# Optimization experiments

Measured on AMD Instinct MI355X. Metric: run time of the kernel, lower is better.

## Reference

```python
import jax, jax.numpy as jnp
import numpy as np

B, S, D, H = 2, 2048, 2048, 16
HD = D // H  # 128


def _rope_tables(seq_len, half_dim, theta=10000.0):
    freqs = 1.0 / (theta ** (np.arange(0, half_dim, dtype=np.float32) / half_dim))
    t = np.arange(seq_len, dtype=np.float32)
    ang = np.outer(t, freqs)  # [S, HD//2]
    return jnp.asarray(np.cos(ang)), jnp.asarray(np.sin(ang))


def setup_inputs() -> dict:
    key = jax.random.key(0)
    kx, kq, kk, kv, ko = jax.random.split(key, 5)
    cos, sin = _rope_tables(S, HD // 2)
    return {
        "x": jax.random.normal(kx, (B, S, D), dtype=jnp.float32),
        "cos": cos,  # [S, HD//2]
        "sin": sin,  # [S, HD//2]
        "wq": jax.random.normal(kq, (D, D), dtype=jnp.float32) * 0.02,
        "wk": jax.random.normal(kk, (D, D), dtype=jnp.float32) * 0.02,
        "wv": jax.random.normal(kv, (D, D), dtype=jnp.float32) * 0.02,
        "wo": jax.random.normal(ko, (D, D), dtype=jnp.float32) * 0.02,
    }


def _apply_rotary(t, cos, sin):
    # t: [B, S, H, HD]; rotate consecutive pairs (complex multiply)
    t2 = t.reshape(*t.shape[:-1], HD // 2, 2)
    te, to = t2[..., 0], t2[..., 1]
    c = cos[None, :, None, :]
    s = sin[None, :, None, :]
    out = jnp.stack([te * c - to * s, te * s + to * c], axis=-1)
    return out.reshape(t.shape)


def reference(x, cos, sin, wq, wk, wv, wo):
    xq = (x @ wq).reshape(B, S, H, HD)
    xk = (x @ wk).reshape(B, S, H, HD)
    xv = (x @ wv).reshape(B, S, H, HD)
    # FAITHFUL to source: rotary applied to xq and xv (NOT xk)
    xq = _apply_rotary(xq, cos, sin)
    xv = _apply_rotary(xv, cos, sin)
    q = xq.transpose(0, 2, 1, 3)  # [B,H,S,HD]
    k = xk.transpose(0, 2, 1, 3)
    v = xv.transpose(0, 2, 1, 3)
    scores = jnp.einsum("bhqd,bhkd->bhqk", q, k) / jnp.sqrt(jnp.float32(HD))
    mask = jnp.triu(jnp.full((S, S), -jnp.inf, dtype=scores.dtype), k=1)
    scores = scores + mask[None, None, :, :]
    probs = jax.nn.softmax(scores, axis=-1)
    out = jnp.einsum("bhqk,bhkd->bhqd", probs, v)  # [B,H,S,HD]
    out = out.transpose(0, 2, 1, 3).reshape(B, S, D)
    return out @ wo
```

## Files before the change

### kernel.cpp

```cpp
#include <hip/hip_runtime.h>
#include <hip/hip_bf16.h>

typedef short short8 __attribute__((ext_vector_type(8)));
typedef float f32x4 __attribute__((ext_vector_type(4)));
typedef int int4v __attribute__((ext_vector_type(4)));

#define B_ 2
#define S_ 2048
#define D_ 2048
#define H_ 16
#define HD_ 128
#define K_ 2048

#define GLL16(gp, lp) __builtin_amdgcn_global_load_lds( \
    (const __attribute__((address_space(1))) void*)(gp), \
    (__attribute__((address_space(3))) void*)(lp), 16, 0, 0)

__device__ inline ushort f2bf(float f) {
    union { float f; unsigned u; } v; v.f = f;
    unsigned r = v.u + 0x7FFFu + ((v.u >> 16) & 1u);
    return (ushort)(r >> 16);
}
__device__ inline float bf2f(ushort b) {
    union { unsigned u; float f; } v; v.u = ((unsigned)b) << 16;
    return v.f;
}

__global__ void cast_kernel(const float* __restrict__ src, ushort* __restrict__ dst, int n4) {
    int i = blockIdx.x * blockDim.x + threadIdx.x;
    if (i >= n4) return;
    float4 v = reinterpret_cast<const float4*>(src)[i];
    ushort4 o;
    o.x = f2bf(v.x); o.y = f2bf(v.y); o.z = f2bf(v.z); o.w = f2bf(v.w);
    reinterpret_cast<ushort4*>(dst)[i] = o;
}

__global__ __launch_bounds__(256) void cast_transpose4(
        const float* __restrict__ s0, const float* __restrict__ s1,
        const float* __restrict__ s2, const float* __restrict__ s3,
        ushort* __restrict__ d0, ushort* __restrict__ d1,
        ushort* __restrict__ d2, ushort* __restrict__ d3) {
    __shared__ ushort tile[64][72];
    const int z = blockIdx.z;
    const float* src = (z == 0) ? s0 : (z == 1) ? s1 : (z == 2) ? s2 : s3;
    ushort* dst = (z == 0) ? d0 : (z == 1) ? d1 : (z == 2) ? d2 : d3;
    const int bk = blockIdx.y * 64, bn = blockIdx.x * 64;
    const int t = threadIdx.x;
    #pragma unroll
    for (int it = 0; it < 4; ++it) {
        int id = t + it * 256;
        int row = id >> 4;
        int c4 = (id & 15) * 4;
        float4 v = *reinterpret_cast<const float4*>(&src[(size_t)(bk + row) * D_ + bn + c4]);
        ushort4 o; o.x = f2bf(v.x); o.y = f2bf(v.y); o.z = f2bf(v.z); o.w = f2bf(v.w);
        *reinterpret_cast<ushort4*>(&tile[row][c4]) = o;
    }
    __syncthreads();
    #pragma unroll
    for (int it = 0; it < 4; ++it) {
        int id = t + it * 256;
        int n = id >> 4;
        int c4 = (id & 15) * 4;
        ushort4 o;
        o.x = tile[c4 + 0][n]; o.y = tile[c4 + 1][n];
        o.z = tile[c4 + 2][n]; o.w = tile[c4 + 3][n];
        *reinterpret_cast<ushort4*>(&dst[(size_t)(bn + n) * D_ + bk + c4]) = o;
    }
}

__global__ void rope_kernel(ushort* __restrict__ t, const float* __restrict__ cosT,
                            const float* __restrict__ sinT, int npairs) {
    int pid = blockIdx.x * blockDim.x + threadIdx.x;
    if (pid >= npairs) return;
    int i = pid & 63;
    int s = (pid >> 6) & (S_ - 1);
    unsigned pr = reinterpret_cast<unsigned*>(t)[pid];
    float e = bf2f((ushort)(pr & 0xFFFFu));
    float o = bf2f((ushort)(pr >> 16));
    float c = cosT[s * 64 + i];
    float sn = sinT[s * 64 + i];
    float oe = e * c - o * sn;
    float oo = e * sn + o * c;
    unsigned outp = ((unsigned)f2bf(oo) << 16) | (unsigned)f2bf(oe);
    reinterpret_cast<unsigned*>(t)[pid] = outp;
}

#define BAR8() __builtin_amdgcn_s_barrier()
#define VMC1() asm volatile("s_waitcnt vmcnt(1)" ::: "memory")
#define VMC0() asm volatile("s_waitcnt vmcnt(0)" ::: "memory")

template<int MODE>
__global__ __launch_bounds__(512, 2) void gemm8(const ushort* __restrict__ A,
        const ushort* __restrict__ Bt, ushort* __restrict__ q0, ushort* __restrict__ k0,
        ushort* __restrict__ v0, float* __restrict__ outf, int nbx) {
    constexpr int NC      = (MODE == 0) ? 3 : 2;
    constexpr int BN      = (MODE == 0) ? 192 : 128;
    constexpr int WCOLS   = BN / 4;
    constexpr int BBYTES  = BN * 128;
    constexpr int BSTRIDE = 32768 + BBYTES;

    extern __shared__ char smem[];
    const int tid = threadIdx.x, lane = tid & 63, wv = tid >> 6;
    const int wm = wv >> 2, wn = wv & 3;
    const int l15 = lane & 15, lg = lane >> 4;
    const int nwg = (int)gridDim.x, cpx = nwg >> 3;
    const int swzb = ((int)blockIdx.x & 7) * cpx + ((int)blockIdx.x >> 3);
    const int bn = (swzb % nbx) * BN, bm = (swzb / nbx) * 256;

    f32x4 acc[8][NC] = {};

    const int grl = wv * 8 + (lane >> 3);
    const int swc = (((lane & 7) ^ ((lane >> 3) & 7)) * 8);
    const ushort* Ag = A + (size_t)(bm + grl) * K_ + swc;
    const ushort* Bg = Bt + (size_t)(bn + grl) * K_ + swc;
    const size_t rowHA = (size_t)128 * K_;
    const size_t row64 = (size_t)64 * K_;

#define STAGE_A(t, h) do { if ((t) < 32) { \
        const ushort* g = Ag + (size_t)(h) * rowHA + (size_t)(t) * 64; \
        char* l = smem + (((t) & 1) ? BSTRIDE : 0) + ((h) << 14) + (wv << 10); \
        GLL16(g, l); GLL16(g + row64, l + 8192); } } while (0)
#define STAGE_B(t, ch) do { if ((t) < 32) { \
        const ushort* g = Bg + (size_t)(ch) * row64 + (size_t)(t) * 64; \
        char* l = smem + (((t) & 1) ? BSTRIDE : 0) + 32768 + (ch) * 8192 + (wv << 10); \
        GLL16(g, l); } } while (0)
#define STAGE_B_HI(t) do { STAGE_B(t, 1); if (MODE == 0) STAGE_B(t, 2); } while (0)

    const int colsw0 = (lg * 16) ^ ((l15 & 7) << 4);
    const int colsw1 = (64 + lg * 16) ^ ((l15 & 7) << 4);
    const char* abase0 = smem + (wm << 14);
    const char* bbase0 = smem + 32768;
    const char* abase1 = abase0 + BSTRIDE;
    const char* bbase1 = bbase0 + BSTRIDE;

#define LDA(ab, q, cs) do { _Pragma("unroll") for (int f = 0; f < 4; ++f) \
        a[f] = *reinterpret_cast<const short8*>((ab) + ((q) * 64 + f * 16 + l15) * 128 + (cs)); } while (0)
#define LDB(bb, cs) do { _Pragma("unroll") for (int c = 0; c < NC; ++c) { \
        const int rw = wn * WCOLS + c * 16; \
        b[c] = *reinterpret_cast<const short8*>((bb) + (rw >> 6) * 8192 + ((rw & 63) + l15) * 128 + (cs)); } } while (0)
#define MM(q) do { __builtin_amdgcn_s_setprio(1); \
        _Pragma("unroll") for (int f = 0; f < 4; ++f) \
        _Pragma("unroll") for (int c = 0; c < NC; ++c) \
            acc[(q) * 4 + f][c] = __builtin_amdgcn_mfma_f32_16x16x32_bf16(a[f], b[c], acc[(q) * 4 + f][c], 0, 0, 0); \
        __builtin_amdgcn_s_setprio(0); } while (0)

    STAGE_A(0, 0); STAGE_A(0, 1);
    STAGE_B(0, 0); STAGE_B_HI(0);
    STAGE_B(1, 0);
    VMC1();
    BAR8();

    for (int i = 0; i < 16; ++i) {
        const int t1 = 2 * i + 1, s0 = 2 * i + 2, s1 = 2 * i + 3;
        short8 a[4], b[NC];
        LDB(bbase0, colsw0); LDA(abase0, 0, colsw0);
        STAGE_A(t1, 0);
        BAR8(); MM(0); BAR8();
        LDA(abase0, 1, colsw0);
        STAGE_A(t1, 1);
        BAR8(); MM(1); BAR8();
        LDB(bbase0, colsw1); LDA(abase0, 0, colsw1);
        STAGE_B_HI(t1);
        BAR8(); MM(0); BAR8();
        LDA(abase0, 1, colsw1);
        STAGE_B(s0, 0);
        if (s0 < 32) VMC1(); else VMC0();
        BAR8(); MM(1); BAR8();
        LDB(bbase1, colsw0); LDA(abase1, 0, colsw0);
        STAGE_A(s0, 0);
        BAR8(); MM(0); BAR8();
        LDA(abase1, 1, colsw0);
        STAGE_A(s0, 1);
        BAR8(); MM(1); BAR8();
        LDB(bbase1, colsw1); LDA(abase1, 0, colsw1);
        STAGE_B_HI(s0);
        BAR8(); MM(0); BAR8();
        LDA(abase1, 1, colsw1);
        STAGE_B(s1, 0);
        if (s1 < 32) VMC1(); else VMC0();
        BAR8(); MM(1); BAR8();
    }

    if (MODE == 0) {
        #pragma unroll
        for (int c = 0; c < NC; ++c) {
            const int col0 = bn + wn * WCOLS + c * 16;
            const int seg = col0 >> 11;
            ushort* segp = (seg == 0) ? q0 : ((seg == 1) ? k0 : v0);
            const int col = col0 + l15;
            const int h = (col >> 7) & (H_ - 1), d = col & (HD_ - 1);
            #pragma unroll
            for (int rf = 0; rf < 8; ++rf)
                #pragma unroll
                for (int j = 0; j < 4; ++j) {
                    int row = bm + wm * 128 + rf * 16 + lg * 4 + j;
                    int bb = row >> 11, s = row & (S_ - 1);
                    segp[(((size_t)(bb * H_ + h)) * S_ + s) * HD_ + d] = f2bf(acc[rf][c][j]);
                }
        }
    } else {
        #pragma unroll
        for (int rf = 0; rf < 8; ++rf)
            #pragma unroll
            for (int c = 0; c < NC; ++c)
                #pragma unroll
                for (int j = 0; j < 4; ++j) {
                    int row = bm + wm * 128 + rf * 16 + lg * 4 + j;
                    int col = bn + wn * WCOLS + c * 16 + l15;
                    outf[(size_t)row * D_ + col] = acc[rf][c][j];
                }
    }
#undef STAGE_A
#undef STAGE_B
#undef STAGE_B_HI
#undef LDA
#undef LDB
#undef MM
}

__global__ __launch_bounds__(512, 4) void attn5(const ushort* __restrict__ Qm,
        const ushort* __restrict__ Km, const ushort* __restrict__ Vm,
        ushort* __restrict__ Om) {
    __shared__ __align__(16) ushort Kb[2][64 * 128];
    __shared__ __align__(16) ushort Vt[2][128][72];
    const int tid = threadIdx.x, lane = tid & 63, wv = tid >> 6;
    const int l15 = lane & 15, lg = lane >> 4;
    const int yy = (int)blockIdx.y;
    const int qt = (yy < 8) ? (15 - 2 * yy) : (2 * (yy - 8));
    const int bh = blockIdx.x;
    const size_t base = (size_t)bh * S_ * HD_;
    const int qrow0 = qt * 128 + wv * 16;
    const float C = 0.1275174f;

    short8 qf[4];
    {
        const ushort* qp = Qm + base + (size_t)(qrow0 + l15) * HD_;
        #pragma unroll
        for (int c = 0; c < 4; ++c)
            qf[c] = *reinterpret_cast<const short8*>(qp + c * 32 + lg * 8);
    }
    f32x4 oacc[8] = {};
    float mS = -1e30f, lS = 0.f;
    const int ntiles = 2 * qt + 2;
    const int kmask0 = 2 * qt + (wv >> 2);

    {
        #pragma unroll
        for (int c = 0; c < 2; ++c) {
            int row = wv * 8 + c * 4 + (lane >> 4);
            GLL16(Km + base + (size_t)row * HD_ + (((lane & 15) ^ (row & 7)) << 3),
                  &Kb[0][wv * 1024 + c * 512]);
        }
        const ushort* vp = Vm + base + (size_t)lane * HD_ + wv * 16;
        #pragma unroll
        for (int cc = 0; cc < 2; ++cc) {
            int4v v = *reinterpret_cast<const int4v*>(vp + cc * 8);
            const ushort* e = reinterpret_cast<const ushort*>(&v);
            #pragma unroll
            for (int j = 0; j < 8; ++j) Vt[0][wv * 16 + cc * 8 + j][lane] = e[j];
        }
    }
    __syncthreads();

    int cur = 0;
    for (int kt = 0; kt < ntiles; ++kt) {
        const bool pfn = (kt + 1 < ntiles);
        int4v vr[2];
        if (pfn) {
            const int r0 = (kt + 1) * 64;
            #pragma unroll
            for (int c = 0; c < 2; ++c) {
                int row = wv * 8 + c * 4 + (lane >> 4);
                GLL16(Km + base + (size_t)(r0 + row) * HD_ + (((lane & 15) ^ (row & 7)) << 3),
                      &Kb[cur ^ 1][wv * 1024 + c * 512]);
            }
            const ushort* vp = Vm + base + (size_t)(r0 + lane) * HD_ + wv * 16;
            #pragma unroll
            for (int cc = 0; cc < 2; ++cc)
                vr[cc] = *reinterpret_cast<const int4v*>(vp + cc * 8);
        }
        f32x4 sacc[4] = {};
        const ushort* Kc = &Kb[cur][0];
        __builtin_amdgcn_s_setprio(1);
        #pragma unroll
        for (int ct = 0; ct < 4; ++ct) {
            const int row = ct * 16 + l15;
            const int sw = (row & 7) << 3;
            #pragma unroll
            for (int c = 0; c < 4; ++c) {
                short8 kf = *reinterpret_cast<const short8*>(
                    Kc + row * 128 + ((c * 32 + lg * 8) ^ sw));
                sacc[ct] = __builtin_amdgcn_mfma_f32_16x16x32_bf16(kf, qf[c], sacc[ct], 0, 0, 0);
            }
        }
        __builtin_amdgcn_s_setprio(0);

        float t16[16];
        #pragma unroll
        for (int ct = 0; ct < 4; ++ct)
            #pragma unroll
            for (int j = 0; j < 4; ++j) t16[ct * 4 + j] = sacc[ct][j];
        if (kt >= kmask0) {
            const int thr = qrow0 + l15 - kt * 64;
            #pragma unroll
            for (int ct = 0; ct < 4; ++ct)
                #pragma unroll
                for (int j = 0; j < 4; ++j)
                    if (ct * 16 + lg * 4 + j > thr) t16[ct * 4 + j] = -1e30f;
        }
        float mx[8];
        #pragma unroll
        for (int i = 0; i < 8; ++i) mx[i] = fmaxf(t16[i], t16[i + 8]);
        #pragma unroll
        for (int i = 0; i < 4; ++i) mx[i] = fmaxf(mx[i], mx[i + 4]);
        float m64 = fmaxf(fmaxf(mx[0], mx[1]), fmaxf(mx[2], mx[3]));
        m64 = fmaxf(m64, __shfl_xor(m64, 16));
        m64 = fmaxf(m64, __shfl_xor(m64, 32));
        if (!__all(m64 - mS <= 47.0f)) {
            float mnew = fmaxf(mS, m64);
            float corr = __builtin_amdgcn_exp2f((mS - mnew) * C);
            lS *= corr;
            #pragma unroll
            for (int dt = 0; dt < 8; ++dt)
                #pragma unroll
                for (int j = 0; j < 4; ++j) oacc[dt][j] *= corr;
            mS = mnew;
        }
        const float mcc = mS * C;
        float p[16];
        #pragma unroll
        for (int i = 0; i < 16; ++i)
            p[i] = __builtin_amdgcn_exp2f(fmaf(t16[i], C, -mcc));
        float sm[8];
        #pragma unroll
        for (int i = 0; i < 8; ++i) sm[i] = p[i] + p[i + 8];
        #pragma unroll
        for (int i = 0; i < 4; ++i) sm[i] = sm[i] + sm[i + 4];
        float psum = (sm[0] + sm[1]) + (sm[2] + sm[3]);
        psum += __shfl_xor(psum, 16);
        psum += __shfl_xor(psum, 32);
        lS += psum;

        unsigned dw[8];
        #pragma unroll
        for (int ct = 0; ct < 4; ++ct)
            #pragma unroll
            for (int u = 0; u < 2; ++u) {
                __hip_bfloat162 h2 = __float22bfloat162_rn(
                    float2{p[ct * 4 + 2 * u], p[ct * 4 + 2 * u + 1]});
                dw[ct * 2 + u] = *reinterpret_cast<unsigned*>(&h2);
            }
        #pragma unroll
        for (int c2 = 0; c2 < 2; ++c2) {
            int4v pfd;
            #pragma unroll
            for (int d = 0; d < 4; ++d) {
                int srcl = (lg & 1) * 32 + (d >> 1) * 16 + l15;
                int r0 = __shfl((int)dw[(2 * c2) * 2 + (d & 1)], srcl);
                int r1 = __shfl((int)dw[(2 * c2 + 1) * 2 + (d & 1)], srcl);
                pfd[d] = (lg & 2) ? r1 : r0;
            }
            short8 pf = *reinterpret_cast<short8*>(&pfd);
            __builtin_amdgcn_s_setprio(1);
            #pragma unroll
            for (int dt = 0; dt < 8; ++dt) {
                short8 vf = *reinterpret_cast<const short8*>(
                    &Vt[cur][dt * 16 + l15][c2 * 32 + lg * 8]);
                oacc[dt] = __builtin_amdgcn_mfma_f32_16x16x32_bf16(vf, pf, oacc[dt], 0, 0, 0);
            }
            __builtin_amdgcn_s_setprio(0);
        }
        if (pfn) {
            #pragma unroll
            for (int cc = 0; cc < 2; ++cc) {
                const ushort* e = reinterpret_cast<const ushort*>(&vr[cc]);
                #pragma unroll
                for (int j = 0; j < 8; ++j) Vt[cur ^ 1][wv * 16 + cc * 8 + j][lane] = e[j];
            }
        }
        __syncthreads();
        cur ^= 1;
    }
    const int b = bh >> 4, h = bh & (H_ - 1);
    const int q = qrow0 + l15;
    const float inv = 1.0f / lS;
    ushort* op = Om + ((size_t)(b * S_ + q)) * D_ + h * HD_;
    #pragma unroll
    for (int dt = 0; dt < 8; ++dt) {
        ushort4 o;
        o.x = f2bf(oacc[dt][0] * inv);
        o.y = f2bf(oacc[dt][1] * inv);
        o.z = f2bf(oacc[dt][2] * inv);
        o.w = f2bf(oacc[dt][3] * inv);
        *reinterpret_cast<ushort4*>(op + dt * 16 + lg * 4) = o;
    }
}

extern "C" void kernel_launch(void* const* d_in, const int* in_sizes, int n_in,
                              void* d_out, int out_size, void* d_ws, size_t ws_size,
                              hipStream_t stream) {
    const float* x    = (const float*)d_in[0];
    const float* cosT = (const float*)d_in[1];
    const float* sinT = (const float*)d_in[2];
    const float* wq   = (const float*)d_in[3];
    const float* wk   = (const float*)d_in[4];
    const float* wv   = (const float*)d_in[5];
    const float* wo   = (const float*)d_in[6];
    float* out = (float*)d_out;

    char* ws = (char*)d_ws;
    const size_t szX = (size_t)B_ * S_ * D_ * 2;
    const size_t szW = (size_t)D_ * D_ * 2;
    ushort* xb   = (ushort*)(ws);
    ushort* wcat = (ushort*)(ws + szX);
    ushort* woT  = (ushort*)(ws + szX + 3 * szW);
    ushort* q0   = (ushort*)(ws + szX + 4 * szW);
    ushort* k0   = (ushort*)(ws + szX + 4 * szW + szX);
    ushort* v0   = (ushort*)(ws + szX + 4 * szW + 2 * szX);
    ushort* att  = xb;

    hipFuncSetAttribute(reinterpret_cast<const void*>(&gemm8<0>),
                        hipFuncAttributeMaxDynamicSharedMemorySize, 114688);
    hipFuncSetAttribute(reinterpret_cast<const void*>(&gemm8<1>),
                        hipFuncAttributeMaxDynamicSharedMemorySize, 98304);

    const int nx = B_ * S_ * D_;
    cast_kernel<<<nx / 4 / 256, 256, 0, stream>>>(x, xb, nx / 4);
    cast_transpose4<<<dim3(D_ / 64, D_ / 64, 4), 256, 0, stream>>>(
        wq, wk, wv, wo, wcat, wcat + (size_t)D_ * D_, wcat + 2 * (size_t)D_ * D_, woT);

    gemm8<0><<<512, 512, 114688, stream>>>(xb, wcat, q0, k0, v0, nullptr, 32);

    const int npairs = B_ * S_ * H_ * 64;
    rope_kernel<<<npairs / 256, 256, 0, stream>>>(q0, cosT, sinT, npairs);
    rope_kernel<<<npairs / 256, 256, 0, stream>>>(v0, cosT, sinT, npairs);

    attn5<<<dim3(B_ * H_, S_ / 128), 512, 0, stream>>>(q0, k0, v0, att);

    gemm8<1><<<256, 512, 98304, stream>>>(att, woT, nullptr, nullptr, nullptr, out, 16);
}
```

Baseline: 265.2 us.

## Fuse rotary embedding into attention loads and restage GEMM B-tile prefetch

Removes the two standalone rope kernels and applies the rotary rotation to Q fragments and V tiles as they are loaded inside the attention kernel, reading cos/sin directly. This avoids a full read-modify-write pass over the Q and V tensors plus two kernel launches, at the cost of extra ALU work and cos/sin loads inside attention. The GEMM also changes its prefetch schedule so that all B chunks for a stage are issued together, with the vmcnt wait adjusted per mode.

```diff
diff --git a/kernel.cpp b/kernel.cpp
--- a/kernel.cpp
+++ b/kernel.cpp
@@ -24,6 +24,22 @@
 __device__ inline float bf2f(ushort b) {
     union { unsigned u; float f; } v; v.u = ((unsigned)b) << 16;
     return v.f;
+}
+
+__device__ inline short8 rope8(short8 raw, const float* __restrict__ cosp,
+                               const float* __restrict__ sinp) {
+    float4 cs = *reinterpret_cast<const float4*>(cosp);
+    float4 sn = *reinterpret_cast<const float4*>(sinp);
+    const float* c = reinterpret_cast<const float*>(&cs);
+    const float* s = reinterpret_cast<const float*>(&sn);
+    short8 out;
+    #pragma unroll
+    for (int j = 0; j < 4; ++j) {
+        float a = bf2f((ushort)raw[2 * j]), b = bf2f((ushort)raw[2 * j + 1]);
+        out[2 * j]     = (short)f2bf(fmaf(a, c[j], -(b * s[j])));
+        out[2 * j + 1] = (short)f2bf(fmaf(a, s[j], b * c[j]));
+    }
+    return out;
 }
 
 __global__ void cast_kernel(const float* __restrict__ src, ushort* __restrict__ dst, int n4) {
@@ -68,25 +84,7 @@
     }
 }
 
-__global__ void rope_kernel(ushort* __restrict__ t, const float* __restrict__ cosT,
-                            const float* __restrict__ sinT, int npairs) {
-    int pid = blockIdx.x * blockDim.x + threadIdx.x;
-    if (pid >= npairs) return;
-    int i = pid & 63;
-    int s = (pid >> 6) & (S_ - 1);
-    unsigned pr = reinterpret_cast<unsigned*>(t)[pid];
-    float e = bf2f((ushort)(pr & 0xFFFFu));
-    float o = bf2f((ushort)(pr >> 16));
-    float c = cosT[s * 64 + i];
-    float sn = sinT[s * 64 + i];
-    float oe = e * c - o * sn;
-    float oo = e * sn + o * c;
-    unsigned outp = ((unsigned)f2bf(oo) << 16) | (unsigned)f2bf(oe);
-    reinterpret_cast<unsigned*>(t)[pid] = outp;
-}
-
 #define BAR8() __builtin_amdgcn_s_barrier()
-#define VMC1() asm volatile("s_waitcnt vmcnt(1)" ::: "memory")
 #define VMC0() asm volatile("s_waitcnt vmcnt(0)" ::: "memory")
 
 template<int MODE>
@@ -95,6 +93,7 @@
         ushort* __restrict__ v0, float* __restrict__ outf, int nbx) {
     constexpr int NC      = (MODE == 0) ? 3 : 2;
     constexpr int BN      = (MODE == 0) ? 192 : 128;
+    constexpr int NBCH    = BN / 64;
     constexpr int WCOLS   = BN / 4;
     constexpr int BBYTES  = BN * 128;
     constexpr int BSTRIDE = 32768 + BBYTES;
@@ -116,6 +115,8 @@
     const size_t rowHA = (size_t)128 * K_;
     const size_t row64 = (size_t)64 * K_;
 
+#define VMCN() do { if (MODE == 0) asm volatile("s_waitcnt vmcnt(3)" ::: "memory"); \
+                    else           asm volatile("s_waitcnt vmcnt(2)" ::: "memory"); } while (0)
 #define STAGE_A(t, h) do { if ((t) < 32) { \
         const ushort* g = Ag + (size_t)(h) * rowHA + (size_t)(t) * 64; \
         char* l = smem + (((t) & 1) ? BSTRIDE : 0) + ((h) << 14) + (wv << 10); \
@@ -124,7 +125,8 @@
         const ushort* g = Bg + (size_t)(ch) * row64 + (size_t)(t) * 64; \
         char* l = smem + (((t) & 1) ? BSTRIDE : 0) + 32768 + (ch) * 8192 + (wv << 10); \
         GLL16(g, l); } } while (0)
-#define STAGE_B_HI(t) do { STAGE_B(t, 1); if (MODE == 0) STAGE_B(t, 2); } while (0)
+#define STAGE_B_ALL(t) do { _Pragma("unroll") \
+        for (int ch = 0; ch < NBCH; ++ch) STAGE_B(t, ch); } while (0)
 
     const int colsw0 = (lg * 16) ^ ((l15 & 7) << 4);
     const int colsw1 = (64 + lg * 16) ^ ((l15 & 7) << 4);
@@ -145,9 +147,9 @@
         __builtin_amdgcn_s_setprio(0); } while (0)
 
     STAGE_A(0, 0); STAGE_A(0, 1);
-    STAGE_B(0, 0); STAGE_B_HI(0);
-    STAGE_B(1, 0);
-    VMC1();
+    STAGE_B_ALL(0);
+    STAGE_B_ALL(1);
+    VMCN();
     BAR8();
 
     for (int i = 0; i < 16; ++i) {
@@ -160,11 +162,10 @@
         STAGE_A(t1, 1);
         BAR8(); MM(1); BAR8();
         LDB(bbase0, colsw1); LDA(abase0, 0, colsw1);
-        STAGE_B_HI(t1);
         BAR8(); MM(0); BAR8();
         LDA(abase0, 1, colsw1);
-        STAGE_B(s0, 0);
-        if (s0 < 32) VMC1(); else VMC0();
+        STAGE_B_ALL(s0);
+        if (s0 < 32) VMCN(); else VMC0();
         BAR8(); MM(1); BAR8();
         LDB(bbase1, colsw0); LDA(abase1, 0, colsw0);
         STAGE_A(s0, 0);
@@ -173,11 +174,10 @@
         STAGE_A(s0, 1);
         BAR8(); MM(1); BAR8();
         LDB(bbase1, colsw1); LDA(abase1, 0, colsw1);
-        STAGE_B_HI(s0);
         BAR8(); MM(0); BAR8();
         LDA(abase1, 1, colsw1);
-        STAGE_B(s1, 0);
-        if (s1 < 32) VMC1(); else VMC0();
+        STAGE_B_ALL(s1);
+        if (s1 < 32) VMCN(); else VMC0();
         BAR8(); MM(1); BAR8();
     }
 
@@ -210,17 +210,19 @@
                     outf[(size_t)row * D_ + col] = acc[rf][c][j];
                 }
     }
+#undef VMCN
 #undef STAGE_A
 #undef STAGE_B
-#undef STAGE_B_HI
+#undef STAGE_B_ALL
 #undef LDA
 #undef LDB
 #undef MM
 }
 
-__global__ __launch_bounds__(512, 4) void attn5(const ushort* __restrict__ Qm,
+__global__ __launch_bounds__(512, 4) void attn6(const ushort* __restrict__ Qm,
         const ushort* __restrict__ Km, const ushort* __restrict__ Vm,
-        ushort* __restrict__ Om) {
+        ushort* __restrict__ Om,
+        const float* __restrict__ cosT, const float* __restrict__ sinT) {
     __shared__ __align__(16) ushort Kb[2][64 * 128];
     __shared__ __align__(16) ushort Vt[2][128][72];
     const int tid = threadIdx.x, lane = tid & 63, wv = tid >> 6;
@@ -234,10 +236,15 @@
 
     short8 qf[4];
     {
-        const ushort* qp = Qm + base + (size_t)(qrow0 + l15) * HD_;
-        #pragma unroll
-        for (int c = 0; c < 4; ++c)
-            qf[c] = *reinterpret_cast<const short8*>(qp + c * 32 + lg * 8);
+        const int q = qrow0 + l15;
+        const ushort* qp = Qm + base + (size_t)q * HD_;
+        const float* cq = cosT + (size_t)q * 64;
+        const float* sq = sinT + (size_t)q * 64;
+        #pragma unroll
+        for (int c = 0; c < 4; ++c) {
+            short8 raw = *reinterpret_cast<const short8*>(qp + c * 32 + lg * 8);
+            qf[c] = rope8(raw, cq + c * 16 + lg * 4, sq + c * 16 + lg * 4);
+        }
     }
     f32x4 oacc[8] = {};
     float mS = -1e30f, lS = 0.f;
@@ -252,12 +259,14 @@
                   &Kb[0][wv * 1024 + c * 512]);
         }
         const ushort* vp = Vm + base + (size_t)lane * HD_ + wv * 16;
+        const float* cv = cosT + (size_t)lane * 64 + wv * 8;
+        const float* sv = sinT + (size_t)lane * 64 + wv * 8;
         #pragma unroll
         for (int cc = 0; cc < 2; ++cc) {
-            int4v v = *reinterpret_cast<const int4v*>(vp + cc * 8);
-            const ushort* e = reinterpret_cast<const ushort*>(&v);
-            #pragma unroll
-            for (int j = 0; j < 8; ++j) Vt[0][wv * 16 + cc * 8 + j][lane] = e[j];
+            short8 raw = *reinterpret_cast<const short8*>(vp + cc * 8);
+            short8 r = rope8(raw, cv + cc * 4, sv + cc * 4);
+            #pragma unroll
+            for (int j = 0; j < 8; ++j) Vt[0][wv * 16 + cc * 8 + j][lane] = (ushort)r[j];
         }
     }
     __syncthreads();
@@ -371,11 +380,15 @@
             __builtin_amdgcn_s_setprio(0);
         }
         if (pfn) {
+            const int key = (kt + 1) * 64 + lane;
+            const float* cv = cosT + (size_t)key * 64 + wv * 8;
+            const float* sv = sinT + (size_t)key * 64 + wv * 8;
             #pragma unroll
             for (int cc = 0; cc < 2; ++cc) {
-                const ushort* e = reinterpret_cast<const ushort*>(&vr[cc]);
+                short8 r = rope8(*reinterpret_cast<short8*>(&vr[cc]),
+                                 cv + cc * 4, sv + cc * 4);
                 #pragma unroll
-                for (int j = 0; j < 8; ++j) Vt[cur ^ 1][wv * 16 + cc * 8 + j][lane] = e[j];
+                for (int j = 0; j < 8; ++j) Vt[cur ^ 1][wv * 16 + cc * 8 + j][lane] = (ushort)r[j];
             }
         }
         __syncthreads();
@@ -431,11 +444,7 @@
 
     gemm8<0><<<512, 512, 114688, stream>>>(xb, wcat, q0, k0, v0, nullptr, 32);
 
-    const int npairs = B_ * S_ * H_ * 64;
-    rope_kernel<<<npairs / 256, 256, 0, stream>>>(q0, cosT, sinT, npairs);
-    rope_kernel<<<npairs / 256, 256, 0, stream>>>(v0, cosT, sinT, npairs);
-
-    attn5<<<dim3(B_ * H_, S_ / 128), 512, 0, stream>>>(q0, k0, v0, att);
+    attn6<<<dim3(B_ * H_, S_ / 128), 512, 0, stream>>>(q0, k0, v0, att, cosT, sinT);
 
     gemm8<1><<<256, 512, 98304, stream>>>(att, woT, nullptr, nullptr, nullptr, out, 16);
 }
```

New measurement: 273.5 us. +3.1%, slower.
